# Kernel optimization log

Hardware: AMD Instinct MI355X
Metric: run time of the kernel (lower is better)

## Reference

```python
import jax, jax.numpy as jnp
import numpy as np

B, T, C, H = 4, 4096, 1024, 16

def setup_inputs() -> dict:
    key = jax.random.key(0)
    k1, k2, k3, k4 = jax.random.split(key, 4)
    return {
        "x": jax.random.normal(k1, (B, T, C), dtype=jnp.float32),
        "W_attn": jax.random.normal(k2, (C, C), dtype=jnp.float32) * 0.02,
        "b_attn": jnp.zeros((C,), dtype=jnp.float32),
        "W_proj": jax.random.normal(k3, (C, C), dtype=jnp.float32) * 0.02,
        "b_proj": jnp.zeros((C,), dtype=jnp.float32),
        "temp": jnp.ones((H, 1), dtype=jnp.float32),
        "n_head": H,
    }

def reference(x, W_attn, b_attn, W_proj, b_proj, temp, n_head):
    Bb, Tt, Cc = x.shape
    D = Cc // n_head
    # c_attn (torch Linear: x @ W.T + b)
    w = x @ W_attn.T + b_attn                         # (B,T,C)
    w = w.reshape(Bb, Tt, n_head, D).transpose(0, 2, 1, 3)  # (B,H,T,D)
    # F.normalize over token axis (dim=-2), eps=1e-12
    norm = jnp.maximum(jnp.sqrt(jnp.sum(w * w, axis=-2, keepdims=True)), 1e-12)
    w_normed = w / norm
    tmp = jnp.sum(w_normed ** 2, axis=-1) * temp      # (B,H,T) * (H,1) -> (B,H,T)
    Pi = jax.nn.softmax(tmp, axis=1)                  # softmax over heads
    Pi_prob = Pi / (jnp.sum(Pi, axis=-1, keepdims=True) + 1e-8)  # (B,H,T)
    dots = jnp.einsum('bht,bhtd->bhd', Pi_prob, w ** 2)          # (B,H,D)
    attn = 1.0 / (1.0 + dots)                         # (B,H,D)
    y = -(w * Pi[..., None]) * attn[:, :, None, :]    # (B,H,T,D)
    y = y.transpose(0, 2, 1, 3).reshape(Bb, Tt, Cc)
    return y @ W_proj.T + b_proj
```

## Files before the change

kernel.cpp:

```cpp
#include <hip/hip_runtime.h>
#include <hip/hip_bf16.h>

#define BB 4
#define TT 4096
#define CC 1024
#define HH 16
#define DD 64

typedef __attribute__((ext_vector_type(8))) short short8;
typedef __attribute__((ext_vector_type(8))) __bf16 bf16x8;
typedef __attribute__((ext_vector_type(4))) float f32x4;

static __device__ __forceinline__ unsigned short f2bf(float f) {
    unsigned int u = __builtin_bit_cast(unsigned int, f);
    unsigned int r = (u + 0x7FFFu + ((u >> 16) & 1u)) >> 16;
    return (unsigned short)r;
}

__global__ void k_f32_to_bf16(const float* __restrict__ src,
                              unsigned short* __restrict__ dst, int n4) {
    int i = blockIdx.x * 256 + threadIdx.x;
    if (i >= n4) return;
    float4 v = ((const float4*)src)[i];
    ushort4 o;
    o.x = f2bf(v.x); o.y = f2bf(v.y); o.z = f2bf(v.z); o.w = f2bf(v.w);
    ((ushort4*)dst)[i] = o;
}

#define GBM 256
#define GBN 256
#define GBK 32

static __device__ __forceinline__ void stage_tile32(
    const unsigned short* __restrict__ Gbase, unsigned short* lbase,
    int k0, int K, int wave, int lane)
{
    #pragma unroll
    for (int q = 0; q < 2; ++q) {
        int c = (wave * 2 + q) * 64 + lane;
        int r = c >> 2;
        int j = c & 3;
        int srcj = (j - (r >> 1)) & 3;
        const unsigned short* g = Gbase + (size_t)r * K + k0 + srcj * 8;
        __builtin_amdgcn_global_load_lds(
            (const __attribute__((address_space(1))) void*)g,
            (__attribute__((address_space(3))) void*)(lbase + (wave * 2 + q) * 512),
            16, 0, 0);
    }
}

template<int ACCUM_S>
__global__ __launch_bounds__(512, 2)
void k_gemm256(const unsigned short* __restrict__ A,
               const unsigned short* __restrict__ B,
               const float* __restrict__ bias,
               float* __restrict__ C,
               float* __restrict__ S,
               int M, int N, int K)
{
    __shared__ unsigned short lds[4][16384];
    const int tid  = threadIdx.x;
    const int wave = tid >> 6;
    const int lane = tid & 63;
    const int wr = wave >> 2;
    const int wc = wave & 3;
    const int fr = lane & 15;
    const int hi = lane >> 4;

    const int wg  = blockIdx.x;
    const int swz = (wg & 7) * 32 + (wg >> 3);
    const int bn  = swz & 3;
    const int bm  = swz >> 2;

    const unsigned short* Abase = A + (size_t)(bm * GBM) * K;
    const unsigned short* Bbase = B + (size_t)(bn * GBN) * K;

    const int nt = K / GBK;

    const int sl   = (hi + (fr >> 1)) & 3;
    const int aoff = (wr * 128 + fr) * 32 + sl * 8;
    const int boff = 8192 + (wc * 64 + fr) * 32 + sl * 8;

    f32x4 acc[8][4] = {};

    stage_tile32(Abase, lds[0],        0,       K, wave, lane);
    stage_tile32(Bbase, lds[0] + 8192, 0,       K, wave, lane);
    stage_tile32(Abase, lds[1],        GBK,     K, wave, lane);
    stage_tile32(Bbase, lds[1] + 8192, GBK,     K, wave, lane);
    stage_tile32(Abase, lds[2],        2 * GBK, K, wave, lane);
    stage_tile32(Bbase, lds[2] + 8192, 2 * GBK, K, wave, lane);
    asm volatile("s_waitcnt vmcnt(8)" ::: "memory");
    __builtin_amdgcn_s_barrier();

    for (int kt = 0; kt < nt; ++kt) {
        const unsigned short* buf = lds[kt & 3];
        unsigned short* sbuf = lds[(kt + 3) & 3];
        int k3 = kt + 3; if (k3 >= nt) k3 = nt - 1;

        short8 af0[4], bf0[4];
        #pragma unroll
        for (int i = 0; i < 4; ++i) af0[i] = *(const short8*)&buf[aoff + i * 512];
        #pragma unroll
        for (int i = 0; i < 4; ++i) bf0[i] = *(const short8*)&buf[boff + i * 512];
        stage_tile32(Abase, sbuf, k3 * GBK, K, wave, lane);
        __builtin_amdgcn_s_barrier();
        asm volatile("s_waitcnt lgkmcnt(0)" ::: "memory");
        __builtin_amdgcn_s_setprio(1);
        #pragma unroll
        for (int mi = 0; mi < 4; ++mi)
            #pragma unroll
            for (int ni = 0; ni < 4; ++ni)
                acc[mi][ni] = __builtin_amdgcn_mfma_f32_16x16x32_bf16(
                    __builtin_bit_cast(bf16x8, af0[mi]),
                    __builtin_bit_cast(bf16x8, bf0[ni]),
                    acc[mi][ni], 0, 0, 0);
        __builtin_amdgcn_s_setprio(0);
        __builtin_amdgcn_s_barrier();

        short8 af1[4], bf1[4];
        #pragma unroll
        for (int i = 0; i < 4; ++i) af1[i] = *(const short8*)&buf[aoff + (4 + i) * 512];
        #pragma unroll
        for (int i = 0; i < 4; ++i) bf1[i] = *(const short8*)&buf[boff + i * 512];
        stage_tile32(Bbase, sbuf + 8192, k3 * GBK, K, wave, lane);
        asm volatile("s_waitcnt vmcnt(8)" ::: "memory");
        __builtin_amdgcn_s_barrier();
        asm volatile("s_waitcnt lgkmcnt(0)" ::: "memory");
        __builtin_amdgcn_s_setprio(1);
        #pragma unroll
        for (int mi = 0; mi < 4; ++mi)
            #pragma unroll
            for (int ni = 0; ni < 4; ++ni)
                acc[4 + mi][ni] = __builtin_amdgcn_mfma_f32_16x16x32_bf16(
                    __builtin_bit_cast(bf16x8, af1[mi]),
                    __builtin_bit_cast(bf16x8, bf1[ni]),
                    acc[4 + mi][ni], 0, 0, 0);
        __builtin_amdgcn_s_setprio(0);
        __builtin_amdgcn_s_barrier();
    }

    __syncthreads();

    const int cg = fr;
    const int rg = hi * 4;
    float* sblk = (float*)&lds[0][0];
    if (ACCUM_S) {
        if (tid < GBN) sblk[tid] = 0.f;
        __syncthreads();
    }
    float csum[4] = {};
    #pragma unroll
    for (int mi = 0; mi < 8; ++mi) {
        #pragma unroll
        for (int ni = 0; ni < 4; ++ni) {
            int col = bn * GBN + wc * 64 + ni * 16 + cg;
            float bv = bias[col];
            #pragma unroll
            for (int j = 0; j < 4; ++j) {
                int row = bm * GBM + wr * 128 + mi * 16 + rg + j;
                float v = acc[mi][ni][j] + bv;
                C[(size_t)row * N + col] = v;
                if (ACCUM_S) csum[ni] += v * v;
            }
        }
    }
    if (ACCUM_S) {
        #pragma unroll
        for (int ni = 0; ni < 4; ++ni)
            atomicAdd(&sblk[wc * 64 + ni * 16 + cg], csum[ni]);
        __syncthreads();
        const int b = bm >> 4;
        if (tid < GBN) atomicAdd(&S[b * CC + bn * GBN + tid], sblk[tid]);
    }
}

__global__ __launch_bounds__(256)
void k_row_softmax(const float* __restrict__ w, const float* __restrict__ S,
                   const float* __restrict__ temp,
                   float* __restrict__ Pi, float* __restrict__ dotsU,
                   float* __restrict__ sumPi)
{
    __shared__ float dots_local[CC];
    __shared__ float sPi_local[HH];
    const int tid  = threadIdx.x;
    const int wave = tid >> 6;
    const int lane = tid & 63;
    const int b    = blockIdx.x >> 7;
    const int tile = blockIdx.x & 127;

    for (int c = tid; c < CC; c += 256) dots_local[c] = 0.f;
    if (tid < HH) sPi_local[tid] = 0.f;
    __syncthreads();

    const int g  = lane >> 4;
    const int li = lane & 15;

    float inv[4][4];
    float tsc[4];
    #pragma unroll
    for (int q = 0; q < 4; ++q) {
        int c = q * 256 + lane * 4;
        float4 sv = *(const float4*)&S[b * CC + c];
        inv[q][0] = 1.f / fmaxf(sv.x, 1e-24f);
        inv[q][1] = 1.f / fmaxf(sv.y, 1e-24f);
        inv[q][2] = 1.f / fmaxf(sv.z, 1e-24f);
        inv[q][3] = 1.f / fmaxf(sv.w, 1e-24f);
        tsc[q] = temp[q * 4 + g];
    }

    float dacc[4][4] = {};
    float sPiAcc[4] = {};

    for (int i = 0; i < 8; ++i) {
        int t = tile * 32 + wave * 8 + i;
        const float* row = w + ((size_t)b * TT + t) * CC;
        float4 wv[4];
        float pq[4];
        #pragma unroll
        for (int q = 0; q < 4; ++q) {
            wv[q] = *(const float4*)&row[q * 256 + lane * 4];
            pq[q] = wv[q].x * wv[q].x * inv[q][0] + wv[q].y * wv[q].y * inv[q][1]
                  + wv[q].z * wv[q].z * inv[q][2] + wv[q].w * wv[q].w * inv[q][3];
        }
        #pragma unroll
        for (int off = 1; off < 16; off <<= 1) {
            #pragma unroll
            for (int q = 0; q < 4; ++q) pq[q] += __shfl_xor(pq[q], off);
        }
        float mx = -1e30f;
        #pragma unroll
        for (int q = 0; q < 4; ++q) { pq[q] *= tsc[q]; mx = fmaxf(mx, pq[q]); }
        mx = fmaxf(mx, __shfl_xor(mx, 16));
        mx = fmaxf(mx, __shfl_xor(mx, 32));
        float e[4], ssum = 0.f;
        #pragma unroll
        for (int q = 0; q < 4; ++q) { e[q] = __expf(pq[q] - mx); ssum += e[q]; }
        ssum += __shfl_xor(ssum, 16);
        ssum += __shfl_xor(ssum, 32);
        float rs = 1.f / ssum;
        #pragma unroll
        for (int q = 0; q < 4; ++q) {
            float piq = e[q] * rs;
            dacc[q][0] += piq * wv[q].x * wv[q].x;
            dacc[q][1] += piq * wv[q].y * wv[q].y;
            dacc[q][2] += piq * wv[q].z * wv[q].z;
            dacc[q][3] += piq * wv[q].w * wv[q].w;
            if (li == 0) {
                Pi[((size_t)(b * HH + q * 4 + g)) * TT + t] = piq;
                sPiAcc[q] += piq;
            }
        }
    }

    #pragma unroll
    for (int q = 0; q < 4; ++q) {
        int c = q * 256 + lane * 4;
        atomicAdd(&dots_local[c + 0], dacc[q][0]);
        atomicAdd(&dots_local[c + 1], dacc[q][1]);
        atomicAdd(&dots_local[c + 2], dacc[q][2]);
        atomicAdd(&dots_local[c + 3], dacc[q][3]);
        if (li == 0) atomicAdd(&sPi_local[q * 4 + g], sPiAcc[q]);
    }
    __syncthreads();
    for (int c = tid; c < CC; c += 256) atomicAdd(&dotsU[b * CC + c], dots_local[c]);
    if (tid < HH) atomicAdd(&sumPi[b * HH + tid], sPi_local[tid]);
}

__global__ void k_attnscale(const float* __restrict__ dotsU,
                            const float* __restrict__ sumPi,
                            float* __restrict__ attnScale) {
    int i = blockIdx.x * 256 + threadIdx.x;
    if (i >= BB * CC) return;
    int b = i >> 10;
    int h = (i >> 6) & 15;
    float sp = sumPi[b * HH + h] + 1e-8f;
    attnScale[i] = 1.f / (1.f + dotsU[i] / sp);
}

__global__ void k_make_y(const float* __restrict__ w, const float* __restrict__ Pi,
                         const float* __restrict__ attnScale,
                         unsigned short* __restrict__ y)
{
    size_t i = (size_t)blockIdx.x * 256 + threadIdx.x;
    size_t flat = i * 4;
    int c = (int)(flat & (CC - 1));
    size_t bt = flat >> 10;
    int t = (int)(bt & (TT - 1));
    int b = (int)(bt >> 12);
    int h = c >> 6;
    float pi = Pi[((size_t)(b * HH + h)) * TT + t];
    float4 wv = *(const float4*)&w[flat];
    float4 av = *(const float4*)&attnScale[b * CC + c];
    ushort4 o;
    o.x = f2bf(-(wv.x * pi) * av.x);
    o.y = f2bf(-(wv.y * pi) * av.y);
    o.z = f2bf(-(wv.z * pi) * av.z);
    o.w = f2bf(-(wv.w * pi) * av.w);
    *(ushort4*)&y[flat] = o;
}

extern "C" void kernel_launch(void* const* d_in, const int* in_sizes, int n_in,
                              void* d_out, int out_size, void* d_ws, size_t ws_size,
                              hipStream_t stream) {
    const float* x      = (const float*)d_in[0];
    const float* W_attn = (const float*)d_in[1];
    const float* b_attn = (const float*)d_in[2];
    const float* W_proj = (const float*)d_in[3];
    const float* b_proj = (const float*)d_in[4];
    const float* temp   = (const float*)d_in[5];

    char* ws = (char*)d_ws;
    unsigned short* xy_bf16 = (unsigned short*)(ws);
    unsigned short* Wa_bf16 = (unsigned short*)(ws + 33554432);
    unsigned short* Wp_bf16 = (unsigned short*)(ws + 35651584);
    float* Pi        = (float*)(ws + 37748736);
    float* S         = (float*)(ws + 38797312);
    float* dotsU     = (float*)(ws + 38813696);
    float* sumPi     = (float*)(ws + 38830080);
    float* attnScale = (float*)(ws + 38830336);
    float* wbuf = (float*)d_out;

    k_f32_to_bf16<<<dim3(16384), dim3(256), 0, stream>>>(x, xy_bf16, 4194304);
    k_f32_to_bf16<<<dim3(1024), dim3(256), 0, stream>>>(W_attn, Wa_bf16, 262144);
    k_f32_to_bf16<<<dim3(1024), dim3(256), 0, stream>>>(W_proj, Wp_bf16, 262144);

    hipMemsetAsync(S, 0, 16384 + 16384 + 256, stream);

    k_gemm256<1><<<dim3(256), dim3(512), 0, stream>>>(
        xy_bf16, Wa_bf16, b_attn, wbuf, S, BB * TT, CC, CC);

    k_row_softmax<<<dim3(512), dim3(256), 0, stream>>>(wbuf, S, temp, Pi, dotsU, sumPi);

    k_attnscale<<<dim3(16), dim3(256), 0, stream>>>(dotsU, sumPi, attnScale);

    k_make_y<<<dim3(16384), dim3(256), 0, stream>>>(wbuf, Pi, attnScale, xy_bf16);

    k_gemm256<0><<<dim3(256), dim3(512), 0, stream>>>(
        xy_bf16, Wp_bf16, b_proj, (float*)d_out, nullptr, BB * TT, CC, CC);
}
```

Measured before the change: 152.1 us.

## Fuse x fp32→bf16 conversion into GEMM A-load and store w as bf16

The first GEMM now loads fp32 x directly into LDS with an XOR swizzle and converts to bf16 in registers, which removes the separate x conversion pass. Its output w is written as bf16 instead of fp32, halving the traffic for the softmax and make_y passes, and make_y updates the bf16 buffer in place. The pipeline goes from a 4-stage to a 3-stage LDS ring with a new split of wait counts. Storing w in bf16 loses some precision in the normalization and y, and the fp32 A tile uses more LDS.

Measured after the change: 150.6 us. No clear change (-1.0%).

```diff
diff --git a/kernel.cpp b/kernel.cpp
--- a/kernel.cpp
+++ b/kernel.cpp
@@ -15,6 +15,15 @@
     unsigned int u = __builtin_bit_cast(unsigned int, f);
     unsigned int r = (u + 0x7FFFu + ((u >> 16) & 1u)) >> 16;
     return (unsigned short)r;
+}
+static __device__ __forceinline__ float bf2f(unsigned short h) {
+    return __builtin_bit_cast(float, ((unsigned int)h) << 16);
+}
+static __device__ __forceinline__ bf16x8 cvt8(f32x4 a, f32x4 b) {
+    bf16x8 r;
+    r[0] = (__bf16)a[0]; r[1] = (__bf16)a[1]; r[2] = (__bf16)a[2]; r[3] = (__bf16)a[3];
+    r[4] = (__bf16)b[0]; r[5] = (__bf16)b[1]; r[6] = (__bf16)b[2]; r[7] = (__bf16)b[3];
+    return r;
 }
 
 __global__ void k_f32_to_bf16(const float* __restrict__ src,
@@ -31,7 +40,7 @@
 #define GBN 256
 #define GBK 32
 
-static __device__ __forceinline__ void stage_tile32(
+static __device__ __forceinline__ void stage_b16(
     const unsigned short* __restrict__ Gbase, unsigned short* lbase,
     int k0, int K, int wave, int lane)
 {
@@ -49,102 +58,145 @@
     }
 }
 
-template<int ACCUM_S>
+static __device__ __forceinline__ void stage_a_f32(
+    const float* __restrict__ Gbase, float* lbase,
+    int k0, int K, int wave, int lane)
+{
+    #pragma unroll
+    for (int q = 0; q < 4; ++q) {
+        int c = (wave * 4 + q) * 64 + lane;
+        int r = c >> 3;
+        int s = c & 7;
+        int srcs = s ^ (r & 7);
+        const float* g = Gbase + (size_t)r * K + k0 + srcs * 4;
+        __builtin_amdgcn_global_load_lds(
+            (const __attribute__((address_space(1))) void*)g,
+            (__attribute__((address_space(3))) void*)(lbase + (wave * 4 + q) * 256),
+            16, 0, 0);
+    }
+}
+
+template<int MODE>
 __global__ __launch_bounds__(512, 2)
-void k_gemm256(const unsigned short* __restrict__ A,
-               const unsigned short* __restrict__ B,
+void k_gemm256(const void* __restrict__ Asrc,
+               const unsigned short* __restrict__ Bsrc,
                const float* __restrict__ bias,
-               float* __restrict__ C,
+               void* __restrict__ Cout,
                float* __restrict__ S,
                int M, int N, int K)
 {
-    __shared__ unsigned short lds[4][16384];
+    __shared__ unsigned int Au[3][(MODE == 0) ? 8192 : 4096];
+    __shared__ unsigned short Bl[3][8192];
     const int tid  = threadIdx.x;
     const int wave = tid >> 6;
     const int lane = tid & 63;
-    const int wr = wave >> 2;
-    const int wc = wave & 3;
-    const int fr = lane & 15;
-    const int hi = lane >> 4;
+    const int wr = wave >> 2, wc = wave & 3;
+    const int fr = lane & 15, hi = lane >> 4;
 
     const int wg  = blockIdx.x;
     const int swz = (wg & 7) * 32 + (wg >> 3);
     const int bn  = swz & 3;
     const int bm  = swz >> 2;
-
-    const unsigned short* Abase = A + (size_t)(bm * GBM) * K;
-    const unsigned short* Bbase = B + (size_t)(bn * GBN) * K;
-
-    const int nt = K / GBK;
-
-    const int sl   = (hi + (fr >> 1)) & 3;
-    const int aoff = (wr * 128 + fr) * 32 + sl * 8;
-    const int boff = 8192 + (wc * 64 + fr) * 32 + sl * 8;
+    const int nt  = K / GBK;
+
+    const float* Afg = (const float*)Asrc + (size_t)(bm * GBM) * K;
+    const unsigned short* Abg = (const unsigned short*)Asrc + (size_t)(bm * GBM) * K;
+    const unsigned short* Bbase = Bsrc + (size_t)(bn * GBN) * K;
 
     f32x4 acc[8][4] = {};
 
-    stage_tile32(Abase, lds[0],        0,       K, wave, lane);
-    stage_tile32(Bbase, lds[0] + 8192, 0,       K, wave, lane);
-    stage_tile32(Abase, lds[1],        GBK,     K, wave, lane);
-    stage_tile32(Bbase, lds[1] + 8192, GBK,     K, wave, lane);
-    stage_tile32(Abase, lds[2],        2 * GBK, K, wave, lane);
-    stage_tile32(Bbase, lds[2] + 8192, 2 * GBK, K, wave, lane);
-    asm volatile("s_waitcnt vmcnt(8)" ::: "memory");
+    if (MODE == 0) stage_a_f32(Afg, (float*)Au[0], 0, K, wave, lane);
+    else           stage_b16(Abg, (unsigned short*)Au[0], 0, K, wave, lane);
+    stage_b16(Bbase, Bl[0], 0, K, wave, lane);
+    if (MODE == 0) stage_a_f32(Afg, (float*)Au[1], GBK, K, wave, lane);
+    else           stage_b16(Abg, (unsigned short*)Au[1], GBK, K, wave, lane);
+    stage_b16(Bbase, Bl[1], GBK, K, wave, lane);
+    if (MODE == 0) { asm volatile("s_waitcnt vmcnt(6)" ::: "memory"); }
+    else           { asm volatile("s_waitcnt vmcnt(4)" ::: "memory"); }
     __builtin_amdgcn_s_barrier();
 
+    const int sl    = (hi + (fr >> 1)) & 3;
+    const int boff  = (wc * 64 + fr) * 32 + sl * 8;
+    const int aoffB = (wr * 128 + fr) * 32 + sl * 8;
+    const int sw0   = ((2 * hi)     ^ (fr & 7)) * 4;
+    const int sw1   = ((2 * hi + 1) ^ (fr & 7)) * 4;
+    const int arow  = (wr * 128 + fr) * 32;
+
+    int rb = 0;
     for (int kt = 0; kt < nt; ++kt) {
-        const unsigned short* buf = lds[kt & 3];
-        unsigned short* sbuf = lds[(kt + 3) & 3];
-        int k3 = kt + 3; if (k3 >= nt) k3 = nt - 1;
-
-        short8 af0[4], bf0[4];
-        #pragma unroll
-        for (int i = 0; i < 4; ++i) af0[i] = *(const short8*)&buf[aoff + i * 512];
-        #pragma unroll
-        for (int i = 0; i < 4; ++i) bf0[i] = *(const short8*)&buf[boff + i * 512];
-        stage_tile32(Abase, sbuf, k3 * GBK, K, wave, lane);
+        const int wb = (rb == 0) ? 2 : rb - 1;
+        int ks = kt + 2; if (ks >= nt) ks = nt - 1;
+        const unsigned short* Bc = Bl[rb];
+
+        bf16x8 af0[4]; short8 bfr[4];
+        if (MODE == 0) {
+            const float* Af = (const float*)Au[rb];
+            #pragma unroll
+            for (int mi = 0; mi < 4; ++mi) {
+                f32x4 lo = *(const f32x4*)&Af[arow + mi * 512 + sw0];
+                f32x4 h4 = *(const f32x4*)&Af[arow + mi * 512 + sw1];
+                af0[mi] = cvt8(lo, h4);
+            }
+        } else {
+            const unsigned short* Ab = (const unsigned short*)Au[rb];
+            #pragma unroll
+            for (int mi = 0; mi < 4; ++mi)
+                af0[mi] = __builtin_bit_cast(bf16x8, *(const short8*)&Ab[aoffB + mi * 512]);
+        }
+        #pragma unroll
+        for (int ni = 0; ni < 4; ++ni)
+            bfr[ni] = *(const short8*)&Bc[boff + ni * 512];
+        if (MODE == 0) stage_a_f32(Afg, (float*)Au[wb], ks * GBK, K, wave, lane);
+        else           stage_b16(Abg, (unsigned short*)Au[wb], ks * GBK, K, wave, lane);
+        stage_b16(Bbase, Bl[wb], ks * GBK, K, wave, lane);
         __builtin_amdgcn_s_barrier();
-        asm volatile("s_waitcnt lgkmcnt(0)" ::: "memory");
         __builtin_amdgcn_s_setprio(1);
         #pragma unroll
         for (int mi = 0; mi < 4; ++mi)
             #pragma unroll
             for (int ni = 0; ni < 4; ++ni)
                 acc[mi][ni] = __builtin_amdgcn_mfma_f32_16x16x32_bf16(
-                    __builtin_bit_cast(bf16x8, af0[mi]),
-                    __builtin_bit_cast(bf16x8, bf0[ni]),
-                    acc[mi][ni], 0, 0, 0);
+                    af0[mi], __builtin_bit_cast(bf16x8, bfr[ni]), acc[mi][ni], 0, 0, 0);
         __builtin_amdgcn_s_setprio(0);
         __builtin_amdgcn_s_barrier();
 
-        short8 af1[4], bf1[4];
-        #pragma unroll
-        for (int i = 0; i < 4; ++i) af1[i] = *(const short8*)&buf[aoff + (4 + i) * 512];
-        #pragma unroll
-        for (int i = 0; i < 4; ++i) bf1[i] = *(const short8*)&buf[boff + i * 512];
-        stage_tile32(Bbase, sbuf + 8192, k3 * GBK, K, wave, lane);
-        asm volatile("s_waitcnt vmcnt(8)" ::: "memory");
+        bf16x8 af1[4];
+        if (MODE == 0) {
+            const float* Af = (const float*)Au[rb];
+            #pragma unroll
+            for (int mi = 0; mi < 4; ++mi) {
+                f32x4 lo = *(const f32x4*)&Af[arow + (4 + mi) * 512 + sw0];
+                f32x4 h4 = *(const f32x4*)&Af[arow + (4 + mi) * 512 + sw1];
+                af1[mi] = cvt8(lo, h4);
+            }
+        } else {
+            const unsigned short* Ab = (const unsigned short*)Au[rb];
+            #pragma unroll
+            for (int mi = 0; mi < 4; ++mi)
+                af1[mi] = __builtin_bit_cast(bf16x8, *(const short8*)&Ab[aoffB + (4 + mi) * 512]);
+        }
+        if (MODE == 0) { asm volatile("s_waitcnt vmcnt(6)" ::: "memory"); }
+        else           { asm volatile("s_waitcnt vmcnt(4)" ::: "memory"); }
         __builtin_amdgcn_s_barrier();
-        asm volatile("s_waitcnt lgkmcnt(0)" ::: "memory");
         __builtin_amdgcn_s_setprio(1);
         #pragma unroll
         for (int mi = 0; mi < 4; ++mi)
             #pragma unroll
             for (int ni = 0; ni < 4; ++ni)
                 acc[4 + mi][ni] = __builtin_amdgcn_mfma_f32_16x16x32_bf16(
-                    __builtin_bit_cast(bf16x8, af1[mi]),
-                    __builtin_bit_cast(bf16x8, bf1[ni]),
-                    acc[4 + mi][ni], 0, 0, 0);
+                    af1[mi], __builtin_bit_cast(bf16x8, bfr[ni]), acc[4 + mi][ni], 0, 0, 0);
         __builtin_amdgcn_s_setprio(0);
         __builtin_amdgcn_s_barrier();
+
+        rb = (rb == 2) ? 0 : rb + 1;
     }
 
     __syncthreads();
 
     const int cg = fr;
     const int rg = hi * 4;
-    float* sblk = (float*)&lds[0][0];
-    if (ACCUM_S) {
+    float* sblk = (float*)&Bl[0][0];
+    if (MODE == 0) {
         if (tid < GBN) sblk[tid] = 0.f;
         __syncthreads();
     }
@@ -159,12 +211,16 @@
             for (int j = 0; j < 4; ++j) {
                 int row = bm * GBM + wr * 128 + mi * 16 + rg + j;
                 float v = acc[mi][ni][j] + bv;
-                C[(size_t)row * N + col] = v;
-                if (ACCUM_S) csum[ni] += v * v;
-            }
-        }
-    }
-    if (ACCUM_S) {
+                if (MODE == 0) {
+                    ((unsigned short*)Cout)[(size_t)row * N + col] = f2bf(v);
+                    csum[ni] += v * v;
+                } else {
+                    ((float*)Cout)[(size_t)row * N + col] = v;
+                }
+            }
+        }
+    }
+    if (MODE == 0) {
         #pragma unroll
         for (int ni = 0; ni < 4; ++ni)
             atomicAdd(&sblk[wc * 64 + ni * 16 + cg], csum[ni]);
@@ -175,7 +231,7 @@
 }
 
 __global__ __launch_bounds__(256)
-void k_row_softmax(const float* __restrict__ w, const float* __restrict__ S,
+void k_row_softmax(const unsigned short* __restrict__ w16, const float* __restrict__ S,
                    const float* __restrict__ temp,
                    float* __restrict__ Pi, float* __restrict__ dotsU,
                    float* __restrict__ sumPi)
@@ -185,85 +241,88 @@
     const int tid  = threadIdx.x;
     const int wave = tid >> 6;
     const int lane = tid & 63;
-    const int b    = blockIdx.x >> 7;
+    const int bb   = blockIdx.x >> 7;
     const int tile = blockIdx.x & 127;
 
     for (int c = tid; c < CC; c += 256) dots_local[c] = 0.f;
     if (tid < HH) sPi_local[tid] = 0.f;
     __syncthreads();
 
-    const int g  = lane >> 4;
-    const int li = lane & 15;
-
-    float inv[4][4];
-    float tsc[4];
-    #pragma unroll
-    for (int q = 0; q < 4; ++q) {
-        int c = q * 256 + lane * 4;
-        float4 sv = *(const float4*)&S[b * CC + c];
-        inv[q][0] = 1.f / fmaxf(sv.x, 1e-24f);
-        inv[q][1] = 1.f / fmaxf(sv.y, 1e-24f);
-        inv[q][2] = 1.f / fmaxf(sv.z, 1e-24f);
-        inv[q][3] = 1.f / fmaxf(sv.w, 1e-24f);
-        tsc[q] = temp[q * 4 + g];
-    }
-
-    float dacc[4][4] = {};
-    float sPiAcc[4] = {};
+    const int g3 = lane >> 3;
+    const int li = lane & 7;
+
+    float inv[2][8], tsc[2];
+    #pragma unroll
+    for (int q = 0; q < 2; ++q) {
+        int c = q * 512 + lane * 8;
+        const float4* sp = (const float4*)&S[bb * CC + c];
+        float4 s0 = sp[0], s1 = sp[1];
+        inv[q][0] = 1.f / fmaxf(s0.x, 1e-24f); inv[q][1] = 1.f / fmaxf(s0.y, 1e-24f);
+        inv[q][2] = 1.f / fmaxf(s0.z, 1e-24f); inv[q][3] = 1.f / fmaxf(s0.w, 1e-24f);
+        inv[q][4] = 1.f / fmaxf(s1.x, 1e-24f); inv[q][5] = 1.f / fmaxf(s1.y, 1e-24f);
+        inv[q][6] = 1.f / fmaxf(s1.z, 1e-24f); inv[q][7] = 1.f / fmaxf(s1.w, 1e-24f);
+        tsc[q] = temp[q * 8 + g3];
+    }
+
+    float dacc[2][8] = {};
+    float sPiAcc[2] = {};
 
     for (int i = 0; i < 8; ++i) {
         int t = tile * 32 + wave * 8 + i;
-        const float* row = w + ((size_t)b * TT + t) * CC;
-        float4 wv[4];
-        float pq[4];
-        #pragma unroll
-        for (int q = 0; q < 4; ++q) {
-            wv[q] = *(const float4*)&row[q * 256 + lane * 4];
-            pq[q] = wv[q].x * wv[q].x * inv[q][0] + wv[q].y * wv[q].y * inv[q][1]
-                  + wv[q].z * wv[q].z * inv[q][2] + wv[q].w * wv[q].w * inv[q][3];
-        }
-        #pragma unroll
-        for (int off = 1; off < 16; off <<= 1) {
-            #pragma unroll
-            for (int q = 0; q < 4; ++q) pq[q] += __shfl_xor(pq[q], off);
-        }
-        float mx = -1e30f;
-        #pragma unroll
-        for (int q = 0; q < 4; ++q) { pq[q] *= tsc[q]; mx = fmaxf(mx, pq[q]); }
+        const unsigned short* row = w16 + ((size_t)bb * TT + t) * CC;
+        float wf[2][8];
+        float pq[2];
+        #pragma unroll
+        for (int q = 0; q < 2; ++q) {
+            short8 v = *(const short8*)&row[q * 512 + lane * 8];
+            float s = 0.f;
+            #pragma unroll
+            for (int j = 0; j < 8; ++j) {
+                wf[q][j] = bf2f((unsigned short)v[j]);
+                s += wf[q][j] * wf[q][j] * inv[q][j];
+            }
+            pq[q] = s;
+        }
+        #pragma unroll
+        for (int off = 1; off < 8; off <<= 1) {
+            pq[0] += __shfl_xor(pq[0], off);
+            pq[1] += __shfl_xor(pq[1], off);
+        }
+        pq[0] *= tsc[0]; pq[1] *= tsc[1];
+        float mx = fmaxf(pq[0], pq[1]);
+        mx = fmaxf(mx, __shfl_xor(mx, 8));
         mx = fmaxf(mx, __shfl_xor(mx, 16));
         mx = fmaxf(mx, __shfl_xor(mx, 32));
-        float e[4], ssum = 0.f;
-        #pragma unroll
-        for (int q = 0; q < 4; ++q) { e[q] = __expf(pq[q] - mx); ssum += e[q]; }
-        ssum += __shfl_xor(ssum, 16);
-        ssum += __shfl_xor(ssum, 32);
-        float rs = 1.f / ssum;
-        #pragma unroll
-        for (int q = 0; q < 4; ++q) {
-            float piq = e[q] * rs;
-            dacc[q][0] += piq * wv[q].x * wv[q].x;
-            dacc[q][1] += piq * wv[q].y * wv[q].y;
-            dacc[q][2] += piq * wv[q].z * wv[q].z;
-            dacc[q][3] += piq * wv[q].w * wv[q].w;
+        float e0 = __expf(pq[0] - mx), e1 = __expf(pq[1] - mx);
+        float ss = e0 + e1;
+        ss += __shfl_xor(ss, 8);
+        ss += __shfl_xor(ss, 16);
+        ss += __shfl_xor(ss, 32);
+        float rs = 1.f / ss;
+        float piv[2] = { e0 * rs, e1 * rs };
+        #pragma unroll
+        for (int q = 0; q < 2; ++q) {
+            #pragma unroll
+            for (int j = 0; j < 8; ++j)
+                dacc[q][j] += piv[q] * wf[q][j] * wf[q][j];
             if (li == 0) {
-                Pi[((size_t)(b * HH + q * 4 + g)) * TT + t] = piq;
-                sPiAcc[q] += piq;
-            }
-        }
-    }
-
-    #pragma unroll
-    for (int q = 0; q < 4; ++q) {
-        int c = q * 256 + lane * 4;
-        atomicAdd(&dots_local[c + 0], dacc[q][0]);
-        atomicAdd(&dots_local[c + 1], dacc[q][1]);
-        atomicAdd(&dots_local[c + 2], dacc[q][2]);
-        atomicAdd(&dots_local[c + 3], dacc[q][3]);
-        if (li == 0) atomicAdd(&sPi_local[q * 4 + g], sPiAcc[q]);
+                Pi[((size_t)(bb * HH + q * 8 + g3)) * TT + t] = piv[q];
+                sPiAcc[q] += piv[q];
+            }
+        }
+    }
+
+    #pragma unroll
+    for (int q = 0; q < 2; ++q) {
+        int c = q * 512 + lane * 8;
+        #pragma unroll
+        for (int j = 0; j < 8; ++j)
+            atomicAdd(&dots_local[c + j], dacc[q][j]);
+        if (li == 0) atomicAdd(&sPi_local[q * 8 + g3], sPiAcc[q]);
     }
     __syncthreads();
-    for (int c = tid; c < CC; c += 256) atomicAdd(&dotsU[b * CC + c], dots_local[c]);
-    if (tid < HH) atomicAdd(&sumPi[b * HH + tid], sPi_local[tid]);
+    for (int c = tid; c < CC; c += 256) atomicAdd(&dotsU[bb * CC + c], dots_local[c]);
+    if (tid < HH) atomicAdd(&sumPi[bb * HH + tid], sPi_local[tid]);
 }
 
 __global__ void k_attnscale(const float* __restrict__ dotsU,
@@ -277,26 +336,27 @@
     attnScale[i] = 1.f / (1.f + dotsU[i] / sp);
 }
 
-__global__ void k_make_y(const float* __restrict__ w, const float* __restrict__ Pi,
-                         const float* __restrict__ attnScale,
-                         unsigned short* __restrict__ y)
+__global__ void k_make_y(unsigned short* __restrict__ wy, const float* __restrict__ Pi,
+                         const float* __restrict__ attnScale)
 {
     size_t i = (size_t)blockIdx.x * 256 + threadIdx.x;
-    size_t flat = i * 4;
+    size_t flat = i * 8;
     int c = (int)(flat & (CC - 1));
     size_t bt = flat >> 10;
     int t = (int)(bt & (TT - 1));
     int b = (int)(bt >> 12);
     int h = c >> 6;
     float pi = Pi[((size_t)(b * HH + h)) * TT + t];
-    float4 wv = *(const float4*)&w[flat];
-    float4 av = *(const float4*)&attnScale[b * CC + c];
-    ushort4 o;
-    o.x = f2bf(-(wv.x * pi) * av.x);
-    o.y = f2bf(-(wv.y * pi) * av.y);
-    o.z = f2bf(-(wv.z * pi) * av.z);
-    o.w = f2bf(-(wv.w * pi) * av.w);
-    *(ushort4*)&y[flat] = o;
+    short8 wv = *(const short8*)&wy[flat];
+    f32x4 a0 = *(const f32x4*)&attnScale[b * CC + c];
+    f32x4 a1 = *(const f32x4*)&attnScale[b * CC + c + 4];
+    short8 o;
+    #pragma unroll
+    for (int j = 0; j < 4; ++j) {
+        o[j]     = (short)f2bf(-(bf2f((unsigned short)wv[j])     * pi) * a0[j]);
+        o[4 + j] = (short)f2bf(-(bf2f((unsigned short)wv[4 + j]) * pi) * a1[j]);
+    }
+    *(short8*)&wy[flat] = o;
 }
 
 extern "C" void kernel_launch(void* const* d_in, const int* in_sizes, int n_in,
@@ -310,31 +370,29 @@
     const float* temp   = (const float*)d_in[5];
 
     char* ws = (char*)d_ws;
-    unsigned short* xy_bf16 = (unsigned short*)(ws);
-    unsigned short* Wa_bf16 = (unsigned short*)(ws + 33554432);
-    unsigned short* Wp_bf16 = (unsigned short*)(ws + 35651584);
+    unsigned short* w16  = (unsigned short*)(ws);
+    unsigned short* Wa16 = (unsigned short*)(ws + 33554432);
+    unsigned short* Wp16 = (unsigned short*)(ws + 35651584);
     float* Pi        = (float*)(ws + 37748736);
     float* S         = (float*)(ws + 38797312);
     float* dotsU     = (float*)(ws + 38813696);
     float* sumPi     = (float*)(ws + 38830080);
     float* attnScale = (float*)(ws + 38830336);
-    float* wbuf = (float*)d_out;
-
-    k_f32_to_bf16<<<dim3(16384), dim3(256), 0, stream>>>(x, xy_bf16, 4194304);
-    k_f32_to_bf16<<<dim3(1024), dim3(256), 0, stream>>>(W_attn, Wa_bf16, 262144);
-    k_f32_to_bf16<<<dim3(1024), dim3(256), 0, stream>>>(W_proj, Wp_bf16, 262144);
+
+    k_f32_to_bf16<<<dim3(1024), dim3(256), 0, stream>>>(W_attn, Wa16, 262144);
+    k_f32_to_bf16<<<dim3(1024), dim3(256), 0, stream>>>(W_proj, Wp16, 262144);
 
     hipMemsetAsync(S, 0, 16384 + 16384 + 256, stream);
 
+    k_gemm256<0><<<dim3(256), dim3(512), 0, stream>>>(
+        x, Wa16, b_attn, w16, S, BB * TT, CC, CC);
+
+    k_row_softmax<<<dim3(512), dim3(256), 0, stream>>>(w16, S, temp, Pi, dotsU, sumPi);
+
+    k_attnscale<<<dim3(16), dim3(256), 0, stream>>>(dotsU, sumPi, attnScale);
+
+    k_make_y<<<dim3(8192), dim3(256), 0, stream>>>(w16, Pi, attnScale);
+
     k_gemm256<1><<<dim3(256), dim3(512), 0, stream>>>(
-        xy_bf16, Wa_bf16, b_attn, wbuf, S, BB * TT, CC, CC);
-
-    k_row_softmax<<<dim3(512), dim3(256), 0, stream>>>(wbuf, S, temp, Pi, dotsU, sumPi);
-
-    k_attnscale<<<dim3(16), dim3(256), 0, stream>>>(dotsU, sumPi, attnScale);
-
-    k_make_y<<<dim3(16384), dim3(256), 0, stream>>>(wbuf, Pi, attnScale, xy_bf16);
-
-    k_gemm256<0><<<dim3(256), dim3(512), 0, stream>>>(
-        xy_bf16, Wp_bf16, b_proj, (float*)d_out, nullptr, BB * TT, CC, CC);
-}
+        w16, Wp16, b_proj, d_out, nullptr, BB * TT, CC, CC);
+}
```
